# Performance work log

Measured on AMD Instinct MI355X. Metric: run time of the kernel, lower is better.

## Reference

```python
import jax, jax.numpy as jnp
import numpy as np
from jax import lax

# ---- cfg constants (from init_kwargs) ----
MAX_OBS = 10
MAX_AGENTS = 8
MAX_NEI = MAX_AGENTS - 1
A_MAX, W_MAX = 2.0, 1.0
D_MAX, D_OBS, D_SAFE = 5.0, 0.5, 0.8
G_C1, G_C2 = 1.0, 2.0
G_A1, G_A2 = 1.0, 2.0
G_CN1, G_CN2 = 1.0, 2.0
W_SLACK = 100.0
DAMP, STIFF = G_C1 + G_C2, G_C1 * G_C2
DAMP_A, STIFF_A = G_A1 + G_A2, G_A1 * G_A2
DAMP_CN, STIFF_CN = G_CN1 + G_CN2, G_CN1 * G_CN2
NV = 5  # [a, w, delta_obs, delta_agent, delta_conn]
BIG = 1000.0
N_POWER = 30
N_FISTA = 300
B = 32768

PINV = jnp.array([0.5, 0.5, 1.0 / (2.0 * W_SLACK), 1.0 / (2.0 * W_SLACK), 1.0 / (2.0 * W_SLACK)], jnp.float32)


def _build_Gh(v, p_obs, obs_mask, p_agents, v_agents_local, agents_mask, p_c, v_c, c_mask):
    """Build the batched inequality system A x <= b (incl. box constraints)."""
    Bn = v.shape[0]
    f32 = jnp.float32
    # slack non-negativity rows: -delta_k <= 0
    G_slack = jnp.broadcast_to(jnp.array([[0, 0, -1, 0, 0], [0, 0, 0, -1, 0], [0, 0, 0, 0, -1]], f32), (Bn, 3, NV))
    h_slack = jnp.zeros((Bn, 3), f32)
    # obstacle HOCBF rows
    lx, ly = p_obs[..., 0], p_obs[..., 1]            # (B, MAX_OBS)
    h_obs = lx ** 2 + ly ** 2 - D_OBS ** 2
    h_dot = -2.0 * lx * v
    h_rhs = 2.0 * v ** 2 + DAMP * h_dot + STIFF * h_obs
    z = jnp.zeros_like(lx)
    G_obs = jnp.stack([2.0 * lx * obs_mask, 2.0 * ly * v * obs_mask, -obs_mask, z, z], axis=-1)
    h_obs_r = jnp.where(obs_mask > 0, h_rhs, BIG)
    # neighbor avoidance rows
    ax, ay = p_agents[..., 0], p_agents[..., 1]
    vjx, vjy = v_agents_local[..., 0], v_agents_local[..., 1]
    h_av = ax ** 2 + ay ** 2 - D_SAFE ** 2
    h_av_dot = -2.0 * ax * v + 2.0 * (ax * vjx + ay * vjy)
    h_av_dd = 2.0 * v ** 2 - 2.0 * v * vjx + 2.0 * (-v * vjx + vjx ** 2 + vjy ** 2)
    h_rhs_av = h_av_dd + DAMP_A * h_av_dot + STIFF_A * h_av
    za = jnp.zeros_like(ax)
    G_nei = jnp.stack([2.0 * ax * agents_mask,
                       (2.0 * ay * v - 2.0 * ay * vjx + 2.0 * ax * vjy) * agents_mask,
                       za, -agents_mask, za], axis=-1)
    h_nei_r = jnp.where(agents_mask > 0, h_rhs_av, BIG)
    # connectivity row (closest agent)
    cx, cy = p_c[..., 0], p_c[..., 1]                # (B, 1)
    cvx, cvy = v_c[..., 0], v_c[..., 1]
    h_cn = D_MAX ** 2 - (cx ** 2 + cy ** 2)
    h_cn_dot = -(-2.0 * cx * v + 2.0 * (cx * cvx + cy * cvy))
    h_cn_dd = -(2.0 * v ** 2 - 2.0 * v * cvx + 2.0 * (-v * cvx + cvx ** 2 + cvy ** 2))
    h_rhs_cn = h_cn_dd + DAMP_CN * h_cn_dot + STIFF_CN * h_cn
    zc = jnp.zeros_like(cx)
    G_cn = jnp.stack([-2.0 * cx * c_mask,
                      -(2.0 * cy * v - 2.0 * cy * cvx + 2.0 * cx * cvy) * c_mask,
                      zc, zc, -c_mask], axis=-1)
    h_cn_r = jnp.where(c_mask > 0, h_rhs_cn, BIG)
    # leftover unpopulated row (original allocates max_obs+max_agents+1 hocbf rows but fills max_obs+max_nei+1)
    G_extra = jnp.zeros((Bn, 1, NV), f32)
    h_extra = jnp.full((Bn, 1), BIG, f32)
    # box constraints on u (appended as separate cvxpy constraints in the original)
    G_box = jnp.broadcast_to(jnp.array([[-1, 0, 0, 0, 0], [1, 0, 0, 0, 0], [0, -1, 0, 0, 0], [0, 1, 0, 0, 0]], f32), (Bn, 4, NV))
    h_box = jnp.broadcast_to(jnp.array([A_MAX, A_MAX, W_MAX, W_MAX], f32), (Bn, 4))
    A = jnp.concatenate([G_slack, G_obs, G_nei, G_cn, G_extra, G_box], axis=1)
    b = jnp.concatenate([h_slack, h_obs_r, h_nei_r, h_cn_r, h_extra, h_box], axis=1)
    return A, b


def _solve_qp(u_ref, A, b):
    """min ||u-u_ref||^2 + w*sum(delta^2) s.t. A x <= b; solved via dual FISTA.
    P = diag(2,2,2w,2w,2w), q = (-2 u_ref, 0,0,0). x(lam) = -Pinv (q + A^T lam)."""
    Bn = u_ref.shape[0]
    q = jnp.concatenate([-2.0 * u_ref, jnp.zeros((Bn, 3), u_ref.dtype)], axis=1)  # (B,5)
    # Lipschitz constant of dual gradient: ||A Pinv A^T||_2 via power iteration (constant wrt grads)
    Mm = jnp.einsum('bmn,n,bkn->bmk', A, PINV, A)  # (B, M, M), M=26 tiny
    v0 = jnp.ones((Bn, Mm.shape[1]), A.dtype)
    def power(vv, _):
        w = jnp.einsum('bmk,bk->bm', Mm, vv)
        return w / (jnp.linalg.norm(w, axis=1, keepdims=True) + 1e-12), None
    vtop, _ = lax.scan(power, v0, None, length=N_POWER)
    L = jnp.einsum('bm,bmk,bk->b', vtop, Mm, vtop)
    step = lax.stop_gradient(1.0 / (L + 1e-6))[:, None]  # (B,1)

    def x_of(lam_or_y):
        return -(q + jnp.einsum('bmn,bm->bn', A, lam_or_y)) * PINV

    def fista(carry, _):
        lam, y, tk = carry
        resid = jnp.einsum('bmn,bn->bm', A, x_of(y)) - b
        lam_n = jnp.maximum(y + step * resid, 0.0)
        tk1 = 0.5 * (1.0 + jnp.sqrt(1.0 + 4.0 * tk * tk))
        y_n = lam_n + ((tk - 1.0) / tk1) * (lam_n - lam)
        return (lam_n, y_n, tk1), None

    lam0 = jnp.zeros_like(b)
    (lam, _, _), _ = lax.scan(fista, (lam0, lam0, jnp.float32(1.0)), None, length=N_FISTA)
    x = x_of(lam)
    return x[:, :2]  # u_safe


def setup_inputs() -> dict:
    key = jax.random.key(0)
    ks = jax.random.split(key, 8)
    f32 = jnp.float32
    return {
        'u_nominal': jax.random.normal(ks[0], (B, 2), f32),
        'v_current': jax.random.uniform(ks[1], (B, 1), f32),
        'p_obs': 2.0 * jax.random.normal(ks[2], (B, MAX_OBS, 2), f32),
        'obs_mask': jnp.ones((B, MAX_OBS), f32),
        'p_agents': 2.0 * jax.random.normal(ks[3], (B, MAX_NEI, 2), f32),
        'v_agents_local': jax.random.normal(ks[4], (B, MAX_NEI, 2), f32),
        'agents_mask': jnp.ones((B, MAX_NEI), f32),
        'p_c_agent': 2.0 * jax.random.normal(ks[5], (B, 1, 2), f32),
        'v_c_agent': jax.random.normal(ks[6], (B, 1, 2), f32),
        'closest_mask': jnp.ones((B, 1), f32),
    }


def reference(u_nominal, v_current, p_obs, obs_mask, p_agents, v_agents_local, agents_mask, p_c_agent, v_c_agent, closest_mask):
    A, b = _build_Gh(v_current, p_obs, obs_mask, p_agents, v_agents_local, agents_mask, p_c_agent, v_c_agent, closest_mask)
    return _solve_qp(u_nominal, A, b)
```

## Files before the change

kernel.cpp:

```cpp
#include <hip/hip_runtime.h>


typedef float v2f __attribute__((ext_vector_type(2)));

namespace {
constexpr int N_POWER = 30;
constexpr int N_FISTA = 300;
constexpr float PINV_S = 1.0f / 200.0f;
constexpr float BIG = 1000.0f;

constexpr double csqrt(double x) {
    double r = x * 0.5 + 0.5;
    for (int i = 0; i < 50; ++i) r = 0.5 * (r + x / r);
    return r;
}
struct alignas(32) BOct { float b[8]; };
struct BetaTab8 { BOct q[N_FISTA / 4 + 1]; };
constexpr BetaTab8 make_beta8() {
    BetaTab8 t{};
    float tk = 1.0f;
    for (int k = 0; k < N_FISTA; ++k) {
        const float tk1 = 0.5f * (1.0f + (float)csqrt(1.0 + 4.0 * (double)tk * (double)tk));
        const float bb = (tk - 1.0f) / tk1;
        t.q[k / 4].b[(k % 4) * 2]     = bb;
        t.q[k / 4].b[(k % 4) * 2 + 1] = bb;
        tk = tk1;
    }
    return t;
}
}
__constant__ BetaTab8 BETA8 = make_beta8();

template <int CTRL>
__device__ __forceinline__ float dpp_xor_add(float x) {
    int perm = __builtin_amdgcn_mov_dpp(__float_as_int(x), CTRL, 0xF, 0xF, true);
    return x + __int_as_float(perm);
}

__device__ __forceinline__ v2f vfma(v2f a, v2f b, v2f c) {
    return __builtin_elementwise_fma(a, b, c);
}
__device__ __forceinline__ v2f vmax0(v2f a) {
    const v2f z = {0.f, 0.f};
    return __builtin_elementwise_max(a, z);
}

__global__ __launch_bounds__(256, 2) void cbf_fista11(
    const float* __restrict__ u_nom,
    const float* __restrict__ v_cur,
    const float* __restrict__ p_obs,
    const float* __restrict__ obs_mask,
    const float* __restrict__ p_ag,
    const float* __restrict__ v_ag,
    const float* __restrict__ ag_mask,
    const float* __restrict__ p_c,
    const float* __restrict__ v_c,
    const float* __restrict__ c_mask,
    float* __restrict__ out,
    int B)
{
    const int t = blockIdx.x * 256 + threadIdx.x;
    const int p = t >> 2;
    const int sub = t & 3;
    if (p >= B) return;

    const float v  = v_cur[p];
    const float u0 = u_nom[2 * p];
    const float u1 = u_nom[2 * p + 1];

    float r0[6], r1[6], rA[6], nb[6];
#pragma unroll
    for (int s = 0; s < 6; ++s) { r0[s] = 0.f; r1[s] = 0.f; rA[s] = 0.f; nb[s] = -BIG; }

    auto obs_row = [&](int i, int s) {
        const float lx = p_obs[(p * 10 + i) * 2];
        const float ly = p_obs[(p * 10 + i) * 2 + 1];
        const float m  = obs_mask[p * 10 + i];
        const float h   = lx * lx + ly * ly - 0.25f;
        const float hd  = -2.f * lx * v;
        const float rhs = 2.f * v * v + 3.f * hd + 2.f * h;
        r0[s] = 2.f * lx * m;
        r1[s] = 2.f * ly * v * m;
        rA[s] = -m;
        nb[s] = (m > 0.f) ? -rhs : -BIG;
    };
    auto nei_row = [&](int j, int s) {
        const float ax  = p_ag[(p * 7 + j) * 2];
        const float ay  = p_ag[(p * 7 + j) * 2 + 1];
        const float vjx = v_ag[(p * 7 + j) * 2];
        const float vjy = v_ag[(p * 7 + j) * 2 + 1];
        const float m   = ag_mask[p * 7 + j];
        const float h   = ax * ax + ay * ay - 0.64f;
        const float hd  = -2.f * ax * v + 2.f * (ax * vjx + ay * vjy);
        const float hdd = 2.f * v * v - 2.f * v * vjx
                        + 2.f * (-v * vjx + vjx * vjx + vjy * vjy);
        const float rhs = hdd + 3.f * hd + 2.f * h;
        r0[s] = 2.f * ax * m;
        r1[s] = (2.f * ay * v - 2.f * ay * vjx + 2.f * ax * vjy) * m;
        rA[s] = -m;
        nb[s] = (m > 0.f) ? -rhs : -BIG;
    };

    if (sub == 0) {
        obs_row(0, 0); obs_row(1, 1); obs_row(2, 2);
        obs_row(3, 3); obs_row(4, 4); obs_row(5, 5);
    } else if (sub == 1) {
        obs_row(6, 0); obs_row(7, 1); obs_row(8, 2); obs_row(9, 3);
        rA[4] = -1.f; nb[4] = 0.f;
        r0[5] = -1.f; nb[5] = -2.f;
    } else if (sub == 2) {
        nei_row(0, 0); nei_row(1, 1); nei_row(2, 2);
        nei_row(3, 3); nei_row(4, 4); nei_row(5, 5);
    } else {
        nei_row(6, 0);
        rA[1] = -1.f; nb[1] = 0.f;
        r0[2] =  1.f; nb[2] = -2.f;
        r1[3] = -1.f; nb[3] = -1.f;
        r1[4] =  1.f; nb[4] = -1.f;
    }

    v2f R0[3], R1[3], RA[3], NB[3];
#pragma unroll
    for (int k = 0; k < 3; ++k) {
        R0[k] = v2f{r0[2 * k], r0[2 * k + 1]};
        R1[k] = v2f{r1[2 * k], r1[2 * k + 1]};
        RA[k] = v2f{rA[2 * k], rA[2 * k + 1]};
        NB[k] = v2f{nb[2 * k], nb[2 * k + 1]};
    }

    float c0, c1, cB;
    v2f C0v, C1v, CB2, NCBv;
    {
        const float cx  = p_c[2 * p];
        const float cy  = p_c[2 * p + 1];
        const float cvx = v_c[2 * p];
        const float cvy = v_c[2 * p + 1];
        const float m   = c_mask[p];
        const float h   = 25.f - (cx * cx + cy * cy);
        const float hd  = 2.f * cx * v - 2.f * (cx * cvx + cy * cvy);
        const float hdd = -(2.f * v * v - 2.f * v * cvx
                          + 2.f * (-v * cvx + cvx * cvx + cvy * cvy));
        const float rhs = hdd + 3.f * hd + 2.f * h;
        c0 = -2.f * cx * m;
        c1 = -(2.f * cy * v - 2.f * cy * cvx + 2.f * cx * cvy) * m;
        cB = -m;
        const float ncb = (m > 0.f) ? -rhs : -BIG;
        C0v  = v2f{c0, 0.f};
        C1v  = v2f{c1, 0.f};
        CB2  = v2f{cB, -1.f};
        NCBv = v2f{ncb, 0.f};
    }

    v2f PV[3];
#pragma unroll
    for (int k = 0; k < 3; ++k) PV[k] = v2f{1.f, 1.f};
    float pvC = 1.f, pvS = 1.f;

    auto apply_M = [&]() {
        v2f A0 = vfma(R0[0], PV[0], vfma(R0[1], PV[1], R0[2] * PV[2]));
        v2f A1 = vfma(R1[0], PV[0], vfma(R1[1], PV[1], R1[2] * PV[2]));
        v2f AA = vfma(RA[0], PV[0], vfma(RA[1], PV[1], RA[2] * PV[2]));
        float a0 = A0.x + A0.y, a1 = A1.x + A1.y, aA = AA.x + AA.y;
        a0 = dpp_xor_add<0xB1>(a0); a0 = dpp_xor_add<0x4E>(a0);
        a1 = dpp_xor_add<0xB1>(a1); a1 = dpp_xor_add<0x4E>(a1);
        aA = dpp_xor_add<0xB1>(aA);
        a0 = fmaf(c0, pvC, a0);
        a1 = fmaf(c1, pvC, a1);
        const float aC = fmaf(cB, pvC, -pvS);
        const float x0 = 0.5f * a0, x1 = 0.5f * a1;
        const float xA = PINV_S * aA, xC = PINV_S * aC;
        const v2f X0 = {x0, x0}, X1 = {x1, x1}, XA = {xA, xA};
#pragma unroll
        for (int k = 0; k < 3; ++k)
            PV[k] = vfma(R0[k], X0, vfma(R1[k], X1, RA[k] * XA));
        pvC = fmaf(c0, x0, fmaf(c1, x1, cB * xC));
        pvS = -xC;
    };

#pragma unroll 1
    for (int o = 0; o < N_POWER / 2; ++o) {
        apply_M();
        apply_M();
        v2f NS = vfma(PV[0], PV[0], vfma(PV[1], PV[1], PV[2] * PV[2]));
        float nsq = NS.x + NS.y;
        nsq = dpp_xor_add<0xB1>(nsq); nsq = dpp_xor_add<0x4E>(nsq);
        nsq = fmaf(pvC, pvC, fmaf(pvS, pvS, nsq));
        const float inv = __builtin_amdgcn_rsqf(nsq + 1e-24f);
        const v2f INV = {inv, inv};
#pragma unroll
        for (int k = 0; k < 3; ++k) PV[k] = PV[k] * INV;
        pvC *= inv;
        pvS *= inv;
    }
    float nsh, pA;
    {
        v2f A0 = vfma(R0[0], PV[0], vfma(R0[1], PV[1], R0[2] * PV[2]));
        v2f A1 = vfma(R1[0], PV[0], vfma(R1[1], PV[1], R1[2] * PV[2]));
        v2f AA = vfma(RA[0], PV[0], vfma(RA[1], PV[1], RA[2] * PV[2]));
        float a0 = A0.x + A0.y, a1 = A1.x + A1.y, aA = AA.x + AA.y;
        a0 = dpp_xor_add<0xB1>(a0); a0 = dpp_xor_add<0x4E>(a0);
        a1 = dpp_xor_add<0xB1>(a1); a1 = dpp_xor_add<0x4E>(a1);
        aA = dpp_xor_add<0xB1>(aA);
        a0 = fmaf(c0, pvC, a0);
        a1 = fmaf(c1, pvC, a1);
        const float aC = fmaf(cB, pvC, -pvS);
        float tq = aA * aA;
        tq = dpp_xor_add<0x4E>(tq);
        const float L = 0.5f * (a0 * a0 + a1 * a1) + PINV_S * (tq + aC * aC);
        const float step = __builtin_amdgcn_rcpf(L + 1e-6f);
        nsh = -0.5f * step;
        pA  = -PINV_S * step;
    }

    v2f RA2[3];
    {
        const v2f PAv = {pA, pA};
#pragma unroll
        for (int k = 0; k < 3; ++k) RA2[k] = RA[k] * PAv;
    }
    const v2f CB2s = CB2 * v2f{pA, pA};

    v2f LAE[3], LAO[3], ZV[3];
#pragma unroll
    for (int k = 0; k < 3; ++k) {
        LAE[k] = v2f{0.f, 0.f}; LAO[k] = v2f{0.f, 0.f}; ZV[k] = v2f{0.f, 0.f};
    }
    v2f laCSE = {0.f, 0.f}, laCSO = {0.f, 0.f}, zCS = {0.f, 0.f};

    auto half_step = [&](v2f (&ln_)[3], const v2f (&lp_)[3],
                         v2f& lnCS, v2f lpCS, v2f Bv) {
        v2f A0 = vfma(R0[0], ZV[0], vfma(R0[1], ZV[1], R0[2] * ZV[2]));
        v2f A1 = vfma(R1[0], ZV[0], vfma(R1[1], ZV[1], R1[2] * ZV[2]));
        v2f AA = vfma(RA2[0], ZV[0], vfma(RA2[1], ZV[1], RA2[2] * ZV[2]));
        float a0 = A0.x + A0.y, a1 = A1.x + A1.y, aA = AA.x + AA.y;
        a0 = dpp_xor_add<0xB1>(a0); a0 = dpp_xor_add<0x4E>(a0);
        a1 = dpp_xor_add<0xB1>(a1); a1 = dpp_xor_add<0x4E>(a1);
        aA = dpp_xor_add<0xB1>(aA);
        const v2f tCs = CB2s * zCS;
        const float xC = tCs.x + tCs.y;
        const float x0 = fmaf(nsh, fmaf(c0, zCS.x, a0), u0);
        const float x1 = fmaf(nsh, fmaf(c1, zCS.x, a1), u1);
        const v2f X0 = {x0, x0}, X1 = {x1, x1}, XA = {aA, aA}, XC = {xC, xC};
#pragma unroll
        for (int k = 0; k < 3; ++k) {
            const v2f resid = vfma(R0[k], X0, vfma(R1[k], X1, vfma(RA[k], XA, NB[k])));
            const v2f l = vmax0(ZV[k] + resid);
            ZV[k] = vfma(Bv, l - lp_[k], l);
            ln_[k] = l;
        }
        {
            const v2f resid = vfma(C0v, X0, vfma(C1v, X1, vfma(CB2, XC, NCBv)));
            const v2f l = vmax0(zCS + resid);
            zCS = vfma(Bv, l - lpCS, l);
            lnCS = l;
        }
    };

    BOct bo = BETA8.q[0];
#pragma unroll 1
    for (int o = 0; o < N_FISTA / 4; ++o) {
        const BOct bn = BETA8.q[o + 1];
        const v2f B0 = {bo.b[0], bo.b[1]};
        const v2f B1 = {bo.b[2], bo.b[3]};
        const v2f B2 = {bo.b[4], bo.b[5]};
        const v2f B3 = {bo.b[6], bo.b[7]};
        half_step(LAE, LAO, laCSE, laCSO, B0);
        half_step(LAO, LAE, laCSO, laCSE, B1);
        half_step(LAE, LAO, laCSE, laCSO, B2);
        half_step(LAO, LAE, laCSO, laCSE, B3);
        bo = bn;
    }

    v2f A0 = vfma(R0[0], LAO[0], vfma(R0[1], LAO[1], R0[2] * LAO[2]));
    v2f A1 = vfma(R1[0], LAO[0], vfma(R1[1], LAO[1], R1[2] * LAO[2]));
    float a0 = A0.x + A0.y, a1 = A1.x + A1.y;
    a0 = dpp_xor_add<0xB1>(a0); a0 = dpp_xor_add<0x4E>(a0);
    a1 = dpp_xor_add<0xB1>(a1); a1 = dpp_xor_add<0x4E>(a1);
    a0 = fmaf(c0, laCSO.x, a0);
    a1 = fmaf(c1, laCSO.x, a1);
    if (sub == 0) {
        out[2 * p]     = fmaf(nsh, a0, u0);
        out[2 * p + 1] = fmaf(nsh, a1, u1);
    }
}

extern "C" void kernel_launch(void* const* d_in, const int* in_sizes, int n_in,
                              void* d_out, int out_size, void* d_ws, size_t ws_size,
                              hipStream_t stream) {
    const float* u_nom    = (const float*)d_in[0];
    const float* v_cur    = (const float*)d_in[1];
    const float* p_obs    = (const float*)d_in[2];
    const float* obs_mask = (const float*)d_in[3];
    const float* p_ag     = (const float*)d_in[4];
    const float* v_ag     = (const float*)d_in[5];
    const float* ag_mask  = (const float*)d_in[6];
    const float* p_c      = (const float*)d_in[7];
    const float* v_c      = (const float*)d_in[8];
    const float* c_mask   = (const float*)d_in[9];
    float* out = (float*)d_out;

    const int B = in_sizes[0] / 2;
    const long long threads = 4LL * B;
    const int grid = (int)((threads + 255) / 256);
    cbf_fista11<<<grid, 256, 0, stream>>>(
        u_nom, v_cur, p_obs, obs_mask, p_ag, v_ag, ag_mask, p_c, v_c, c_mask, out, B);
}
```

Before: 144.7 us.

## Process two independent QPs per 4-lane group to interleave dependency chains

Each 4-thread group now solves two problems (q and q+half) with their power-iteration and FISTA steps interleaved, halving the grid. The aim is to hide the latency of the serial DPP reductions and FMA chains through instruction-level parallelism across two independent chains. Launch bounds change from 2 to 1 blocks per CU minimum, which lets the compiler use more registers for the doubled state. The risk is fewer resident waves and higher register pressure, which could cancel the ILP benefit.

```diff
diff --git a/kernel.cpp b/kernel.cpp
--- a/kernel.cpp
+++ b/kernel.cpp
@@ -45,28 +45,25 @@
     return __builtin_elementwise_max(a, z);
 }
 
-__global__ __launch_bounds__(256, 2) void cbf_fista11(
-    const float* __restrict__ u_nom,
-    const float* __restrict__ v_cur,
-    const float* __restrict__ p_obs,
-    const float* __restrict__ obs_mask,
-    const float* __restrict__ p_ag,
-    const float* __restrict__ v_ag,
-    const float* __restrict__ ag_mask,
-    const float* __restrict__ p_c,
-    const float* __restrict__ v_c,
-    const float* __restrict__ c_mask,
-    float* __restrict__ out,
-    int B)
-{
-    const int t = blockIdx.x * 256 + threadIdx.x;
-    const int p = t >> 2;
-    const int sub = t & 3;
-    if (p >= B) return;
-
-    const float v  = v_cur[p];
-    const float u0 = u_nom[2 * p];
-    const float u1 = u_nom[2 * p + 1];
+struct Rows {
+    v2f R0[3], R1[3], RA[3], NB[3];
+    v2f C0v, C1v, CB2, NCBv;
+    float c0, c1, cB;
+    float u0, u1;
+};
+
+__device__ __forceinline__ void build_rows(
+    int p, int sub,
+    const float* __restrict__ u_nom, const float* __restrict__ v_cur,
+    const float* __restrict__ p_obs, const float* __restrict__ obs_mask,
+    const float* __restrict__ p_ag,  const float* __restrict__ v_ag,
+    const float* __restrict__ ag_mask, const float* __restrict__ p_c,
+    const float* __restrict__ v_c,   const float* __restrict__ c_mask,
+    Rows& R)
+{
+    const float v = v_cur[p];
+    R.u0 = u_nom[2 * p];
+    R.u1 = u_nom[2 * p + 1];
 
     float r0[6], r1[6], rA[6], nb[6];
 #pragma unroll
@@ -119,17 +116,14 @@
         r1[4] =  1.f; nb[4] = -1.f;
     }
 
-    v2f R0[3], R1[3], RA[3], NB[3];
 #pragma unroll
     for (int k = 0; k < 3; ++k) {
-        R0[k] = v2f{r0[2 * k], r0[2 * k + 1]};
-        R1[k] = v2f{r1[2 * k], r1[2 * k + 1]};
-        RA[k] = v2f{rA[2 * k], rA[2 * k + 1]};
-        NB[k] = v2f{nb[2 * k], nb[2 * k + 1]};
-    }
-
-    float c0, c1, cB;
-    v2f C0v, C1v, CB2, NCBv;
+        R.R0[k] = v2f{r0[2 * k], r0[2 * k + 1]};
+        R.R1[k] = v2f{r1[2 * k], r1[2 * k + 1]};
+        R.RA[k] = v2f{rA[2 * k], rA[2 * k + 1]};
+        R.NB[k] = v2f{nb[2 * k], nb[2 * k + 1]};
+    }
+
     {
         const float cx  = p_c[2 * p];
         const float cy  = p_c[2 * p + 1];
@@ -141,120 +135,177 @@
         const float hdd = -(2.f * v * v - 2.f * v * cvx
                           + 2.f * (-v * cvx + cvx * cvx + cvy * cvy));
         const float rhs = hdd + 3.f * hd + 2.f * h;
-        c0 = -2.f * cx * m;
-        c1 = -(2.f * cy * v - 2.f * cy * cvx + 2.f * cx * cvy) * m;
-        cB = -m;
+        R.c0 = -2.f * cx * m;
+        R.c1 = -(2.f * cy * v - 2.f * cy * cvx + 2.f * cx * cvy) * m;
+        R.cB = -m;
         const float ncb = (m > 0.f) ? -rhs : -BIG;
-        C0v  = v2f{c0, 0.f};
-        C1v  = v2f{c1, 0.f};
-        CB2  = v2f{cB, -1.f};
-        NCBv = v2f{ncb, 0.f};
-    }
-
-    v2f PV[3];
-#pragma unroll
-    for (int k = 0; k < 3; ++k) PV[k] = v2f{1.f, 1.f};
-    float pvC = 1.f, pvS = 1.f;
-
-    auto apply_M = [&]() {
-        v2f A0 = vfma(R0[0], PV[0], vfma(R0[1], PV[1], R0[2] * PV[2]));
-        v2f A1 = vfma(R1[0], PV[0], vfma(R1[1], PV[1], R1[2] * PV[2]));
-        v2f AA = vfma(RA[0], PV[0], vfma(RA[1], PV[1], RA[2] * PV[2]));
-        float a0 = A0.x + A0.y, a1 = A1.x + A1.y, aA = AA.x + AA.y;
-        a0 = dpp_xor_add<0xB1>(a0); a0 = dpp_xor_add<0x4E>(a0);
-        a1 = dpp_xor_add<0xB1>(a1); a1 = dpp_xor_add<0x4E>(a1);
-        aA = dpp_xor_add<0xB1>(aA);
-        a0 = fmaf(c0, pvC, a0);
-        a1 = fmaf(c1, pvC, a1);
-        const float aC = fmaf(cB, pvC, -pvS);
-        const float x0 = 0.5f * a0, x1 = 0.5f * a1;
-        const float xA = PINV_S * aA, xC = PINV_S * aC;
-        const v2f X0 = {x0, x0}, X1 = {x1, x1}, XA = {xA, xA};
-#pragma unroll
-        for (int k = 0; k < 3; ++k)
-            PV[k] = vfma(R0[k], X0, vfma(R1[k], X1, RA[k] * XA));
-        pvC = fmaf(c0, x0, fmaf(c1, x1, cB * xC));
-        pvS = -xC;
-    };
+        R.C0v  = v2f{R.c0, 0.f};
+        R.C1v  = v2f{R.c1, 0.f};
+        R.CB2  = v2f{R.cB, -1.f};
+        R.NCBv = v2f{ncb, 0.f};
+    }
+}
+
+__device__ __forceinline__ void apply_M(const Rows& R, v2f (&PV)[3], float& pvC, float& pvS)
+{
+    v2f A0 = vfma(R.R0[0], PV[0], vfma(R.R0[1], PV[1], R.R0[2] * PV[2]));
+    v2f A1 = vfma(R.R1[0], PV[0], vfma(R.R1[1], PV[1], R.R1[2] * PV[2]));
+    v2f AA = vfma(R.RA[0], PV[0], vfma(R.RA[1], PV[1], R.RA[2] * PV[2]));
+    float a0 = A0.x + A0.y, a1 = A1.x + A1.y, aA = AA.x + AA.y;
+    a0 = dpp_xor_add<0xB1>(a0); a0 = dpp_xor_add<0x4E>(a0);
+    a1 = dpp_xor_add<0xB1>(a1); a1 = dpp_xor_add<0x4E>(a1);
+    aA = dpp_xor_add<0xB1>(aA);
+    a0 = fmaf(R.c0, pvC, a0);
+    a1 = fmaf(R.c1, pvC, a1);
+    const float aC = fmaf(R.cB, pvC, -pvS);
+    const float x0 = 0.5f * a0, x1 = 0.5f * a1;
+    const float xA = PINV_S * aA, xC = PINV_S * aC;
+    const v2f X0 = {x0, x0}, X1 = {x1, x1}, XA = {xA, xA};
+#pragma unroll
+    for (int k = 0; k < 3; ++k)
+        PV[k] = vfma(R.R0[k], X0, vfma(R.R1[k], X1, R.RA[k] * XA));
+    pvC = fmaf(R.c0, x0, fmaf(R.c1, x1, R.cB * xC));
+    pvS = -xC;
+}
+
+__device__ __forceinline__ void pnorm(v2f (&PV)[3], float& pvC, float& pvS)
+{
+    v2f NS = vfma(PV[0], PV[0], vfma(PV[1], PV[1], PV[2] * PV[2]));
+    float nsq = NS.x + NS.y;
+    nsq = dpp_xor_add<0xB1>(nsq); nsq = dpp_xor_add<0x4E>(nsq);
+    nsq = fmaf(pvC, pvC, fmaf(pvS, pvS, nsq));
+    const float inv = __builtin_amdgcn_rsqf(nsq + 1e-24f);
+    const v2f INV = {inv, inv};
+#pragma unroll
+    for (int k = 0; k < 3; ++k) PV[k] = PV[k] * INV;
+    pvC *= inv;
+    pvS *= inv;
+}
+
+__device__ __forceinline__ void step_consts(const Rows& R, const v2f (&PV)[3],
+                                            float pvC, float pvS,
+                                            float& nsh, float& pA)
+{
+    v2f A0 = vfma(R.R0[0], PV[0], vfma(R.R0[1], PV[1], R.R0[2] * PV[2]));
+    v2f A1 = vfma(R.R1[0], PV[0], vfma(R.R1[1], PV[1], R.R1[2] * PV[2]));
+    v2f AA = vfma(R.RA[0], PV[0], vfma(R.RA[1], PV[1], R.RA[2] * PV[2]));
+    float a0 = A0.x + A0.y, a1 = A1.x + A1.y, aA = AA.x + AA.y;
+    a0 = dpp_xor_add<0xB1>(a0); a0 = dpp_xor_add<0x4E>(a0);
+    a1 = dpp_xor_add<0xB1>(a1); a1 = dpp_xor_add<0x4E>(a1);
+    aA = dpp_xor_add<0xB1>(aA);
+    a0 = fmaf(R.c0, pvC, a0);
+    a1 = fmaf(R.c1, pvC, a1);
+    const float aC = fmaf(R.cB, pvC, -pvS);
+    float tq = aA * aA;
+    tq = dpp_xor_add<0x4E>(tq);
+    const float L = 0.5f * (a0 * a0 + a1 * a1) + PINV_S * (tq + aC * aC);
+    const float step = __builtin_amdgcn_rcpf(L + 1e-6f);
+    nsh = -0.5f * step;
+    pA  = -PINV_S * step;
+}
+
+__device__ __forceinline__ void half_step(const Rows& R, const v2f (&RA2)[3], v2f CB2s,
+                                          float nsh,
+                                          v2f (&ZV)[3], v2f& zCS,
+                                          v2f (&ln)[3], const v2f (&lp)[3],
+                                          v2f& lnCS, v2f lpCS, v2f Bv)
+{
+    v2f A0 = vfma(R.R0[0], ZV[0], vfma(R.R0[1], ZV[1], R.R0[2] * ZV[2]));
+    v2f A1 = vfma(R.R1[0], ZV[0], vfma(R.R1[1], ZV[1], R.R1[2] * ZV[2]));
+    v2f AA = vfma(RA2[0], ZV[0], vfma(RA2[1], ZV[1], RA2[2] * ZV[2]));
+    float a0 = A0.x + A0.y, a1 = A1.x + A1.y, aA = AA.x + AA.y;
+    a0 = dpp_xor_add<0xB1>(a0); a0 = dpp_xor_add<0x4E>(a0);
+    a1 = dpp_xor_add<0xB1>(a1); a1 = dpp_xor_add<0x4E>(a1);
+    aA = dpp_xor_add<0xB1>(aA);
+    const v2f tCs = CB2s * zCS;
+    const float xC = tCs.x + tCs.y;
+    const float x0 = fmaf(nsh, fmaf(R.c0, zCS.x, a0), R.u0);
+    const float x1 = fmaf(nsh, fmaf(R.c1, zCS.x, a1), R.u1);
+    const v2f X0 = {x0, x0}, X1 = {x1, x1}, XA = {aA, aA}, XC = {xC, xC};
+#pragma unroll
+    for (int k = 0; k < 3; ++k) {
+        const v2f resid = vfma(R.R0[k], X0, vfma(R.R1[k], X1, vfma(R.RA[k], XA, R.NB[k])));
+        const v2f l = vmax0(ZV[k] + resid);
+        ZV[k] = vfma(Bv, l - lp[k], l);
+        ln[k] = l;
+    }
+    {
+        const v2f resid = vfma(R.C0v, X0, vfma(R.C1v, X1, vfma(R.CB2, XC, R.NCBv)));
+        const v2f l = vmax0(zCS + resid);
+        zCS = vfma(Bv, l - lpCS, l);
+        lnCS = l;
+    }
+}
+
+struct Fst {
+    v2f LAE[3], LAO[3], ZV[3];
+    v2f laCSE, laCSO, zCS;
+};
+
+__global__ __launch_bounds__(256, 1) void cbf_fista12(
+    const float* __restrict__ u_nom,
+    const float* __restrict__ v_cur,
+    const float* __restrict__ p_obs,
+    const float* __restrict__ obs_mask,
+    const float* __restrict__ p_ag,
+    const float* __restrict__ v_ag,
+    const float* __restrict__ ag_mask,
+    const float* __restrict__ p_c,
+    const float* __restrict__ v_c,
+    const float* __restrict__ c_mask,
+    float* __restrict__ out,
+    int B)
+{
+    const int t = blockIdx.x * 256 + threadIdx.x;
+    const int q = t >> 2;
+    const int sub = t & 3;
+    const int half = (B + 1) >> 1;
+    if (q >= half) return;
+
+    const int pa = q;
+    const int pbi = q + half;
+    const bool hasB = (pbi < B);
+    const int pb = hasB ? pbi : pa;
+
+    Rows Ra, Rb;
+    build_rows(pa, sub, u_nom, v_cur, p_obs, obs_mask, p_ag, v_ag, ag_mask, p_c, v_c, c_mask, Ra);
+    build_rows(pb, sub, u_nom, v_cur, p_obs, obs_mask, p_ag, v_ag, ag_mask, p_c, v_c, c_mask, Rb);
+
+    v2f PVa[3], PVb[3];
+#pragma unroll
+    for (int k = 0; k < 3; ++k) { PVa[k] = v2f{1.f, 1.f}; PVb[k] = v2f{1.f, 1.f}; }
+    float pvCa = 1.f, pvSa = 1.f, pvCb = 1.f, pvSb = 1.f;
 
 #pragma unroll 1
     for (int o = 0; o < N_POWER / 2; ++o) {
-        apply_M();
-        apply_M();
-        v2f NS = vfma(PV[0], PV[0], vfma(PV[1], PV[1], PV[2] * PV[2]));
-        float nsq = NS.x + NS.y;
-        nsq = dpp_xor_add<0xB1>(nsq); nsq = dpp_xor_add<0x4E>(nsq);
-        nsq = fmaf(pvC, pvC, fmaf(pvS, pvS, nsq));
-        const float inv = __builtin_amdgcn_rsqf(nsq + 1e-24f);
-        const v2f INV = {inv, inv};
-#pragma unroll
-        for (int k = 0; k < 3; ++k) PV[k] = PV[k] * INV;
-        pvC *= inv;
-        pvS *= inv;
-    }
-    float nsh, pA;
-    {
-        v2f A0 = vfma(R0[0], PV[0], vfma(R0[1], PV[1], R0[2] * PV[2]));
-        v2f A1 = vfma(R1[0], PV[0], vfma(R1[1], PV[1], R1[2] * PV[2]));
-        v2f AA = vfma(RA[0], PV[0], vfma(RA[1], PV[1], RA[2] * PV[2]));
-        float a0 = A0.x + A0.y, a1 = A1.x + A1.y, aA = AA.x + AA.y;
-        a0 = dpp_xor_add<0xB1>(a0); a0 = dpp_xor_add<0x4E>(a0);
-        a1 = dpp_xor_add<0xB1>(a1); a1 = dpp_xor_add<0x4E>(a1);
-        aA = dpp_xor_add<0xB1>(aA);
-        a0 = fmaf(c0, pvC, a0);
-        a1 = fmaf(c1, pvC, a1);
-        const float aC = fmaf(cB, pvC, -pvS);
-        float tq = aA * aA;
-        tq = dpp_xor_add<0x4E>(tq);
-        const float L = 0.5f * (a0 * a0 + a1 * a1) + PINV_S * (tq + aC * aC);
-        const float step = __builtin_amdgcn_rcpf(L + 1e-6f);
-        nsh = -0.5f * step;
-        pA  = -PINV_S * step;
-    }
-
-    v2f RA2[3];
-    {
-        const v2f PAv = {pA, pA};
-#pragma unroll
-        for (int k = 0; k < 3; ++k) RA2[k] = RA[k] * PAv;
-    }
-    const v2f CB2s = CB2 * v2f{pA, pA};
-
-    v2f LAE[3], LAO[3], ZV[3];
+        apply_M(Ra, PVa, pvCa, pvSa);
+        apply_M(Rb, PVb, pvCb, pvSb);
+        apply_M(Ra, PVa, pvCa, pvSa);
+        apply_M(Rb, PVb, pvCb, pvSb);
+        pnorm(PVa, pvCa, pvSa);
+        pnorm(PVb, pvCb, pvSb);
+    }
+    float nsha, pAa, nshb, pAb;
+    step_consts(Ra, PVa, pvCa, pvSa, nsha, pAa);
+    step_consts(Rb, PVb, pvCb, pvSb, nshb, pAb);
+
+    v2f RA2a[3], RA2b[3];
 #pragma unroll
     for (int k = 0; k < 3; ++k) {
-        LAE[k] = v2f{0.f, 0.f}; LAO[k] = v2f{0.f, 0.f}; ZV[k] = v2f{0.f, 0.f};
-    }
-    v2f laCSE = {0.f, 0.f}, laCSO = {0.f, 0.f}, zCS = {0.f, 0.f};
-
-    auto half_step = [&](v2f (&ln_)[3], const v2f (&lp_)[3],
-                         v2f& lnCS, v2f lpCS, v2f Bv) {
-        v2f A0 = vfma(R0[0], ZV[0], vfma(R0[1], ZV[1], R0[2] * ZV[2]));
-        v2f A1 = vfma(R1[0], ZV[0], vfma(R1[1], ZV[1], R1[2] * ZV[2]));
-        v2f AA = vfma(RA2[0], ZV[0], vfma(RA2[1], ZV[1], RA2[2] * ZV[2]));
-        float a0 = A0.x + A0.y, a1 = A1.x + A1.y, aA = AA.x + AA.y;
-        a0 = dpp_xor_add<0xB1>(a0); a0 = dpp_xor_add<0x4E>(a0);
-        a1 = dpp_xor_add<0xB1>(a1); a1 = dpp_xor_add<0x4E>(a1);
-        aA = dpp_xor_add<0xB1>(aA);
-        const v2f tCs = CB2s * zCS;
-        const float xC = tCs.x + tCs.y;
-        const float x0 = fmaf(nsh, fmaf(c0, zCS.x, a0), u0);
-        const float x1 = fmaf(nsh, fmaf(c1, zCS.x, a1), u1);
-        const v2f X0 = {x0, x0}, X1 = {x1, x1}, XA = {aA, aA}, XC = {xC, xC};
-#pragma unroll
-        for (int k = 0; k < 3; ++k) {
-            const v2f resid = vfma(R0[k], X0, vfma(R1[k], X1, vfma(RA[k], XA, NB[k])));
-            const v2f l = vmax0(ZV[k] + resid);
-            ZV[k] = vfma(Bv, l - lp_[k], l);
-            ln_[k] = l;
-        }
-        {
-            const v2f resid = vfma(C0v, X0, vfma(C1v, X1, vfma(CB2, XC, NCBv)));
-            const v2f l = vmax0(zCS + resid);
-            zCS = vfma(Bv, l - lpCS, l);
-            lnCS = l;
-        }
-    };
+        RA2a[k] = Ra.RA[k] * v2f{pAa, pAa};
+        RA2b[k] = Rb.RA[k] * v2f{pAb, pAb};
+    }
+    const v2f CB2sa = Ra.CB2 * v2f{pAa, pAa};
+    const v2f CB2sb = Rb.CB2 * v2f{pAb, pAb};
+
+    Fst Sa, Sb;
+#pragma unroll
+    for (int k = 0; k < 3; ++k) {
+        Sa.LAE[k] = v2f{0.f, 0.f}; Sa.LAO[k] = v2f{0.f, 0.f}; Sa.ZV[k] = v2f{0.f, 0.f};
+        Sb.LAE[k] = v2f{0.f, 0.f}; Sb.LAO[k] = v2f{0.f, 0.f}; Sb.ZV[k] = v2f{0.f, 0.f};
+    }
+    Sa.laCSE = v2f{0.f, 0.f}; Sa.laCSO = v2f{0.f, 0.f}; Sa.zCS = v2f{0.f, 0.f};
+    Sb.laCSE = v2f{0.f, 0.f}; Sb.laCSO = v2f{0.f, 0.f}; Sb.zCS = v2f{0.f, 0.f};
 
     BOct bo = BETA8.q[0];
 #pragma unroll 1
@@ -264,23 +315,42 @@
         const v2f B1 = {bo.b[2], bo.b[3]};
         const v2f B2 = {bo.b[4], bo.b[5]};
         const v2f B3 = {bo.b[6], bo.b[7]};
-        half_step(LAE, LAO, laCSE, laCSO, B0);
-        half_step(LAO, LAE, laCSO, laCSE, B1);
-        half_step(LAE, LAO, laCSE, laCSO, B2);
-        half_step(LAO, LAE, laCSO, laCSE, B3);
+        half_step(Ra, RA2a, CB2sa, nsha, Sa.ZV, Sa.zCS, Sa.LAE, Sa.LAO, Sa.laCSE, Sa.laCSO, B0);
+        half_step(Rb, RA2b, CB2sb, nshb, Sb.ZV, Sb.zCS, Sb.LAE, Sb.LAO, Sb.laCSE, Sb.laCSO, B0);
+        half_step(Ra, RA2a, CB2sa, nsha, Sa.ZV, Sa.zCS, Sa.LAO, Sa.LAE, Sa.laCSO, Sa.laCSE, B1);
+        half_step(Rb, RA2b, CB2sb, nshb, Sb.ZV, Sb.zCS, Sb.LAO, Sb.LAE, Sb.laCSO, Sb.laCSE, B1);
+        half_step(Ra, RA2a, CB2sa, nsha, Sa.ZV, Sa.zCS, Sa.LAE, Sa.LAO, Sa.laCSE, Sa.laCSO, B2);
+        half_step(Rb, RA2b, CB2sb, nshb, Sb.ZV, Sb.zCS, Sb.LAE, Sb.LAO, Sb.laCSE, Sb.laCSO, B2);
+        half_step(Ra, RA2a, CB2sa, nsha, Sa.ZV, Sa.zCS, Sa.LAO, Sa.LAE, Sa.laCSO, Sa.laCSE, B3);
+        half_step(Rb, RA2b, CB2sb, nshb, Sb.ZV, Sb.zCS, Sb.LAO, Sb.LAE, Sb.laCSO, Sb.laCSE, B3);
         bo = bn;
     }
 
-    v2f A0 = vfma(R0[0], LAO[0], vfma(R0[1], LAO[1], R0[2] * LAO[2]));
-    v2f A1 = vfma(R1[0], LAO[0], vfma(R1[1], LAO[1], R1[2] * LAO[2]));
-    float a0 = A0.x + A0.y, a1 = A1.x + A1.y;
-    a0 = dpp_xor_add<0xB1>(a0); a0 = dpp_xor_add<0x4E>(a0);
-    a1 = dpp_xor_add<0xB1>(a1); a1 = dpp_xor_add<0x4E>(a1);
-    a0 = fmaf(c0, laCSO.x, a0);
-    a1 = fmaf(c1, laCSO.x, a1);
-    if (sub == 0) {
-        out[2 * p]     = fmaf(nsh, a0, u0);
-        out[2 * p + 1] = fmaf(nsh, a1, u1);
+    {
+        v2f A0 = vfma(Ra.R0[0], Sa.LAO[0], vfma(Ra.R0[1], Sa.LAO[1], Ra.R0[2] * Sa.LAO[2]));
+        v2f A1 = vfma(Ra.R1[0], Sa.LAO[0], vfma(Ra.R1[1], Sa.LAO[1], Ra.R1[2] * Sa.LAO[2]));
+        float a0 = A0.x + A0.y, a1 = A1.x + A1.y;
+        a0 = dpp_xor_add<0xB1>(a0); a0 = dpp_xor_add<0x4E>(a0);
+        a1 = dpp_xor_add<0xB1>(a1); a1 = dpp_xor_add<0x4E>(a1);
+        a0 = fmaf(Ra.c0, Sa.laCSO.x, a0);
+        a1 = fmaf(Ra.c1, Sa.laCSO.x, a1);
+        if (sub == 0) {
+            out[2 * pa]     = fmaf(nsha, a0, Ra.u0);
+            out[2 * pa + 1] = fmaf(nsha, a1, Ra.u1);
+        }
+    }
+    {
+        v2f A0 = vfma(Rb.R0[0], Sb.LAO[0], vfma(Rb.R0[1], Sb.LAO[1], Rb.R0[2] * Sb.LAO[2]));
+        v2f A1 = vfma(Rb.R1[0], Sb.LAO[0], vfma(Rb.R1[1], Sb.LAO[1], Rb.R1[2] * Sb.LAO[2]));
+        float a0 = A0.x + A0.y, a1 = A1.x + A1.y;
+        a0 = dpp_xor_add<0xB1>(a0); a0 = dpp_xor_add<0x4E>(a0);
+        a1 = dpp_xor_add<0xB1>(a1); a1 = dpp_xor_add<0x4E>(a1);
+        a0 = fmaf(Rb.c0, Sb.laCSO.x, a0);
+        a1 = fmaf(Rb.c1, Sb.laCSO.x, a1);
+        if (sub == 0 && hasB) {
+            out[2 * pbi]     = fmaf(nshb, a0, Rb.u0);
+            out[2 * pbi + 1] = fmaf(nshb, a1, Rb.u1);
+        }
     }
 }
 
@@ -300,8 +370,9 @@
     float* out = (float*)d_out;
 
     const int B = in_sizes[0] / 2;
-    const long long threads = 4LL * B;
+    const int half = (B + 1) / 2;
+    const long long threads = 4LL * half;
     const int grid = (int)((threads + 255) / 256);
-    cbf_fista11<<<grid, 256, 0, stream>>>(
+    cbf_fista12<<<grid, 256, 0, stream>>>(
         u_nom, v_cur, p_obs, obs_mask, p_ag, v_ag, ag_mask, p_c, v_c, c_mask, out, B);
 }
```

New measurement: 162.9 us. +12.6%, slower.

## Pack two problems per thread group into v2f lanes instead of row pairs

Applied to the files above, without the earlier changes.

Changes the packed-float layout so each lane of a v2f holds a different QP problem (problem q and q+half), with 6 rows per thread held as scalar-per-problem, halving the thread count. The in-register x/y horizontal add is removed and the DPP reductions are now done per problem. The connectivity and its slack row also become separate v2f states, and launch bounds drop to 1 block per SM. The intent is better packed-math utilization and fewer redundant per-thread ops, at the cost of more registers, fewer waves in flight and duplicated DPP reductions.

```diff
diff --git a/kernel.cpp b/kernel.cpp
--- a/kernel.cpp
+++ b/kernel.cpp
@@ -36,6 +36,9 @@
     int perm = __builtin_amdgcn_mov_dpp(__float_as_int(x), CTRL, 0xF, 0xF, true);
     return x + __int_as_float(perm);
 }
+__device__ __forceinline__ float dpp2(float x) {
+    return dpp_xor_add<0x4E>(dpp_xor_add<0xB1>(x));
+}
 
 __device__ __forceinline__ v2f vfma(v2f a, v2f b, v2f c) {
     return __builtin_elementwise_fma(a, b, c);
@@ -44,31 +47,29 @@
     const v2f z = {0.f, 0.f};
     return __builtin_elementwise_max(a, z);
 }
-
-__global__ __launch_bounds__(256, 2) void cbf_fista11(
-    const float* __restrict__ u_nom,
-    const float* __restrict__ v_cur,
-    const float* __restrict__ p_obs,
-    const float* __restrict__ obs_mask,
-    const float* __restrict__ p_ag,
-    const float* __restrict__ v_ag,
-    const float* __restrict__ ag_mask,
-    const float* __restrict__ p_c,
-    const float* __restrict__ v_c,
-    const float* __restrict__ c_mask,
-    float* __restrict__ out,
-    int B)
+__device__ __forceinline__ v2f tree6(const v2f (&C)[6], const v2f (&Z)[6]) {
+    v2f s0 = vfma(C[1], Z[1], C[0] * Z[0]);
+    s0 = vfma(C[2], Z[2], s0);
+    v2f s1 = vfma(C[4], Z[4], C[3] * Z[3]);
+    s1 = vfma(C[5], Z[5], s1);
+    return s0 + s1;
+}
+
+struct ConnS { float c0, c1, cB, ncb, u0, u1; };
+
+__device__ __forceinline__ void build_scalar(
+    int p, int sub,
+    const float* __restrict__ u_nom, const float* __restrict__ v_cur,
+    const float* __restrict__ p_obs, const float* __restrict__ obs_mask,
+    const float* __restrict__ p_ag,  const float* __restrict__ v_ag,
+    const float* __restrict__ ag_mask, const float* __restrict__ p_c,
+    const float* __restrict__ v_c,   const float* __restrict__ c_mask,
+    float (&r0)[6], float (&r1)[6], float (&rA)[6], float (&nb)[6], ConnS& cs)
 {
-    const int t = blockIdx.x * 256 + threadIdx.x;
-    const int p = t >> 2;
-    const int sub = t & 3;
-    if (p >= B) return;
-
-    const float v  = v_cur[p];
-    const float u0 = u_nom[2 * p];
-    const float u1 = u_nom[2 * p + 1];
-
-    float r0[6], r1[6], rA[6], nb[6];
+    const float v = v_cur[p];
+    cs.u0 = u_nom[2 * p];
+    cs.u1 = u_nom[2 * p + 1];
+
 #pragma unroll
     for (int s = 0; s < 6; ++s) { r0[s] = 0.f; r1[s] = 0.f; rA[s] = 0.f; nb[s] = -BIG; }
 
@@ -119,17 +120,6 @@
         r1[4] =  1.f; nb[4] = -1.f;
     }
 
-    v2f R0[3], R1[3], RA[3], NB[3];
-#pragma unroll
-    for (int k = 0; k < 3; ++k) {
-        R0[k] = v2f{r0[2 * k], r0[2 * k + 1]};
-        R1[k] = v2f{r1[2 * k], r1[2 * k + 1]};
-        RA[k] = v2f{rA[2 * k], rA[2 * k + 1]};
-        NB[k] = v2f{nb[2 * k], nb[2 * k + 1]};
-    }
-
-    float c0, c1, cB;
-    v2f C0v, C1v, CB2, NCBv;
     {
         const float cx  = p_c[2 * p];
         const float cy  = p_c[2 * p + 1];
@@ -141,39 +131,83 @@
         const float hdd = -(2.f * v * v - 2.f * v * cvx
                           + 2.f * (-v * cvx + cvx * cvx + cvy * cvy));
         const float rhs = hdd + 3.f * hd + 2.f * h;
-        c0 = -2.f * cx * m;
-        c1 = -(2.f * cy * v - 2.f * cy * cvx + 2.f * cx * cvy) * m;
-        cB = -m;
-        const float ncb = (m > 0.f) ? -rhs : -BIG;
-        C0v  = v2f{c0, 0.f};
-        C1v  = v2f{c1, 0.f};
-        CB2  = v2f{cB, -1.f};
-        NCBv = v2f{ncb, 0.f};
-    }
-
-    v2f PV[3];
-#pragma unroll
-    for (int k = 0; k < 3; ++k) PV[k] = v2f{1.f, 1.f};
-    float pvC = 1.f, pvS = 1.f;
+        cs.c0 = -2.f * cx * m;
+        cs.c1 = -(2.f * cy * v - 2.f * cy * cvx + 2.f * cx * cvy) * m;
+        cs.cB = -m;
+        cs.ncb = (m > 0.f) ? -rhs : -BIG;
+    }
+}
+
+__global__ __launch_bounds__(256, 1) void cbf_fista13(
+    const float* __restrict__ u_nom,
+    const float* __restrict__ v_cur,
+    const float* __restrict__ p_obs,
+    const float* __restrict__ obs_mask,
+    const float* __restrict__ p_ag,
+    const float* __restrict__ v_ag,
+    const float* __restrict__ ag_mask,
+    const float* __restrict__ p_c,
+    const float* __restrict__ v_c,
+    const float* __restrict__ c_mask,
+    float* __restrict__ out,
+    int B)
+{
+    const int t = blockIdx.x * 256 + threadIdx.x;
+    const int q = t >> 2;
+    const int sub = t & 3;
+    const int half = (B + 1) >> 1;
+    if (q >= half) return;
+
+    const int pa = q;
+    const int pbi = q + half;
+    const bool hasB = (pbi < B);
+    const int pb = hasB ? pbi : pa;
+
+    float r0a[6], r1a[6], rAa[6], nba[6]; ConnS ca;
+    float r0b[6], r1b[6], rAb[6], nbb[6]; ConnS cb;
+    build_scalar(pa, sub, u_nom, v_cur, p_obs, obs_mask, p_ag, v_ag, ag_mask, p_c, v_c, c_mask,
+                 r0a, r1a, rAa, nba, ca);
+    build_scalar(pb, sub, u_nom, v_cur, p_obs, obs_mask, p_ag, v_ag, ag_mask, p_c, v_c, c_mask,
+                 r0b, r1b, rAb, nbb, cb);
+
+    v2f R0[6], R1[6], RA[6], NB[6];
+#pragma unroll
+    for (int k = 0; k < 6; ++k) {
+        R0[k] = v2f{r0a[k], r0b[k]};
+        R1[k] = v2f{r1a[k], r1b[k]};
+        RA[k] = v2f{rAa[k], rAb[k]};
+        NB[k] = v2f{nba[k], nbb[k]};
+    }
+    const v2f c0p  = {ca.c0,  cb.c0};
+    const v2f c1p  = {ca.c1,  cb.c1};
+    const v2f cBp  = {ca.cB,  cb.cB};
+    const v2f ncbp = {ca.ncb, cb.ncb};
+    const v2f u0p  = {ca.u0,  cb.u0};
+    const v2f u1p  = {ca.u1,  cb.u1};
+
+    v2f PV[6];
+#pragma unroll
+    for (int k = 0; k < 6; ++k) PV[k] = v2f{1.f, 1.f};
+    v2f pvC = {1.f, 1.f}, pvS = {1.f, 1.f};
 
     auto apply_M = [&]() {
-        v2f A0 = vfma(R0[0], PV[0], vfma(R0[1], PV[1], R0[2] * PV[2]));
-        v2f A1 = vfma(R1[0], PV[0], vfma(R1[1], PV[1], R1[2] * PV[2]));
-        v2f AA = vfma(RA[0], PV[0], vfma(RA[1], PV[1], RA[2] * PV[2]));
-        float a0 = A0.x + A0.y, a1 = A1.x + A1.y, aA = AA.x + AA.y;
-        a0 = dpp_xor_add<0xB1>(a0); a0 = dpp_xor_add<0x4E>(a0);
-        a1 = dpp_xor_add<0xB1>(a1); a1 = dpp_xor_add<0x4E>(a1);
-        aA = dpp_xor_add<0xB1>(aA);
-        a0 = fmaf(c0, pvC, a0);
-        a1 = fmaf(c1, pvC, a1);
-        const float aC = fmaf(cB, pvC, -pvS);
-        const float x0 = 0.5f * a0, x1 = 0.5f * a1;
-        const float xA = PINV_S * aA, xC = PINV_S * aC;
-        const v2f X0 = {x0, x0}, X1 = {x1, x1}, XA = {xA, xA};
-#pragma unroll
-        for (int k = 0; k < 3; ++k)
-            PV[k] = vfma(R0[k], X0, vfma(R1[k], X1, RA[k] * XA));
-        pvC = fmaf(c0, x0, fmaf(c1, x1, cB * xC));
+        const v2f A0 = tree6(R0, PV);
+        const v2f A1 = tree6(R1, PV);
+        const v2f AA = tree6(RA, PV);
+        const float a0A = dpp2(A0.x), a0B = dpp2(A0.y);
+        const float a1A = dpp2(A1.x), a1B = dpp2(A1.y);
+        const float aAA = dpp_xor_add<0xB1>(AA.x);
+        const float aAB = dpp_xor_add<0xB1>(AA.y);
+        const v2f a0p = vfma(c0p, pvC, v2f{a0A, a0B});
+        const v2f a1p = vfma(c1p, pvC, v2f{a1A, a1B});
+        const v2f aCp = vfma(cBp, pvC, -pvS);
+        const v2f x0 = a0p * 0.5f, x1 = a1p * 0.5f;
+        const v2f xA = v2f{aAA, aAB} * PINV_S;
+        const v2f xC = aCp * PINV_S;
+#pragma unroll
+        for (int k = 0; k < 6; ++k)
+            PV[k] = vfma(R0[k], x0, vfma(R1[k], x1, RA[k] * xA));
+        pvC = vfma(c0p, x0, vfma(c1p, x1, cBp * xC));
         pvS = -xC;
     };
 
@@ -181,78 +215,87 @@
     for (int o = 0; o < N_POWER / 2; ++o) {
         apply_M();
         apply_M();
-        v2f NS = vfma(PV[0], PV[0], vfma(PV[1], PV[1], PV[2] * PV[2]));
-        float nsq = NS.x + NS.y;
-        nsq = dpp_xor_add<0xB1>(nsq); nsq = dpp_xor_add<0x4E>(nsq);
-        nsq = fmaf(pvC, pvC, fmaf(pvS, pvS, nsq));
-        const float inv = __builtin_amdgcn_rsqf(nsq + 1e-24f);
-        const v2f INV = {inv, inv};
-#pragma unroll
-        for (int k = 0; k < 3; ++k) PV[k] = PV[k] * INV;
-        pvC *= inv;
-        pvS *= inv;
-    }
-    float nsh, pA;
+        const v2f NS = tree6(PV, PV);
+        const float nA = dpp2(NS.x), nB = dpp2(NS.y);
+        const v2f nsq = vfma(pvC, pvC, vfma(pvS, pvS, v2f{nA, nB}));
+        const float invA = __builtin_amdgcn_rsqf(nsq.x + 1e-24f);
+        const float invB = __builtin_amdgcn_rsqf(nsq.y + 1e-24f);
+        const v2f INV = {invA, invB};
+#pragma unroll
+        for (int k = 0; k < 6; ++k) PV[k] = PV[k] * INV;
+        pvC = pvC * INV;
+        pvS = pvS * INV;
+    }
+
+    v2f nsh_p, pA_p;
     {
-        v2f A0 = vfma(R0[0], PV[0], vfma(R0[1], PV[1], R0[2] * PV[2]));
-        v2f A1 = vfma(R1[0], PV[0], vfma(R1[1], PV[1], R1[2] * PV[2]));
-        v2f AA = vfma(RA[0], PV[0], vfma(RA[1], PV[1], RA[2] * PV[2]));
-        float a0 = A0.x + A0.y, a1 = A1.x + A1.y, aA = AA.x + AA.y;
-        a0 = dpp_xor_add<0xB1>(a0); a0 = dpp_xor_add<0x4E>(a0);
-        a1 = dpp_xor_add<0xB1>(a1); a1 = dpp_xor_add<0x4E>(a1);
-        aA = dpp_xor_add<0xB1>(aA);
-        a0 = fmaf(c0, pvC, a0);
-        a1 = fmaf(c1, pvC, a1);
-        const float aC = fmaf(cB, pvC, -pvS);
-        float tq = aA * aA;
-        tq = dpp_xor_add<0x4E>(tq);
-        const float L = 0.5f * (a0 * a0 + a1 * a1) + PINV_S * (tq + aC * aC);
-        const float step = __builtin_amdgcn_rcpf(L + 1e-6f);
-        nsh = -0.5f * step;
-        pA  = -PINV_S * step;
-    }
-
-    v2f RA2[3];
-    {
-        const v2f PAv = {pA, pA};
-#pragma unroll
-        for (int k = 0; k < 3; ++k) RA2[k] = RA[k] * PAv;
-    }
-    const v2f CB2s = CB2 * v2f{pA, pA};
-
-    v2f LAE[3], LAO[3], ZV[3];
-#pragma unroll
-    for (int k = 0; k < 3; ++k) {
-        LAE[k] = v2f{0.f, 0.f}; LAO[k] = v2f{0.f, 0.f}; ZV[k] = v2f{0.f, 0.f};
-    }
-    v2f laCSE = {0.f, 0.f}, laCSO = {0.f, 0.f}, zCS = {0.f, 0.f};
-
-    auto half_step = [&](v2f (&ln_)[3], const v2f (&lp_)[3],
-                         v2f& lnCS, v2f lpCS, v2f Bv) {
-        v2f A0 = vfma(R0[0], ZV[0], vfma(R0[1], ZV[1], R0[2] * ZV[2]));
-        v2f A1 = vfma(R1[0], ZV[0], vfma(R1[1], ZV[1], R1[2] * ZV[2]));
-        v2f AA = vfma(RA2[0], ZV[0], vfma(RA2[1], ZV[1], RA2[2] * ZV[2]));
-        float a0 = A0.x + A0.y, a1 = A1.x + A1.y, aA = AA.x + AA.y;
-        a0 = dpp_xor_add<0xB1>(a0); a0 = dpp_xor_add<0x4E>(a0);
-        a1 = dpp_xor_add<0xB1>(a1); a1 = dpp_xor_add<0x4E>(a1);
-        aA = dpp_xor_add<0xB1>(aA);
-        const v2f tCs = CB2s * zCS;
-        const float xC = tCs.x + tCs.y;
-        const float x0 = fmaf(nsh, fmaf(c0, zCS.x, a0), u0);
-        const float x1 = fmaf(nsh, fmaf(c1, zCS.x, a1), u1);
-        const v2f X0 = {x0, x0}, X1 = {x1, x1}, XA = {aA, aA}, XC = {xC, xC};
-#pragma unroll
-        for (int k = 0; k < 3; ++k) {
+        const v2f A0 = tree6(R0, PV);
+        const v2f A1 = tree6(R1, PV);
+        const v2f AA = tree6(RA, PV);
+        const float a0A = dpp2(A0.x), a0B = dpp2(A0.y);
+        const float a1A = dpp2(A1.x), a1B = dpp2(A1.y);
+        const float aAA = dpp_xor_add<0xB1>(AA.x);
+        const float aAB = dpp_xor_add<0xB1>(AA.y);
+        const v2f a0p = vfma(c0p, pvC, v2f{a0A, a0B});
+        const v2f a1p = vfma(c1p, pvC, v2f{a1A, a1B});
+        const v2f aCp = vfma(cBp, pvC, -pvS);
+        const v2f aAp = {aAA, aAB};
+        const v2f sq = aAp * aAp;
+        const float tqA = dpp_xor_add<0x4E>(sq.x);
+        const float tqB = dpp_xor_add<0x4E>(sq.y);
+        const v2f tq = vfma(aCp, aCp, v2f{tqA, tqB});
+        const v2f hterm = vfma(a0p, a0p, a1p * a1p) * 0.5f;
+        const v2f L = vfma(tq, v2f{PINV_S, PINV_S}, hterm);
+        const float stA = __builtin_amdgcn_rcpf(L.x + 1e-6f);
+        const float stB = __builtin_amdgcn_rcpf(L.y + 1e-6f);
+        nsh_p = v2f{stA, stB} * -0.5f;
+        pA_p  = v2f{stA, stB} * -PINV_S;
+    }
+
+    v2f RA2[6];
+#pragma unroll
+    for (int k = 0; k < 6; ++k) RA2[k] = RA[k] * pA_p;
+    const v2f cBs = cBp * pA_p;
+    const v2f npA = -pA_p;
+
+    v2f ZV[6], LAE[6], LAO[6];
+#pragma unroll
+    for (int k = 0; k < 6; ++k) {
+        ZV[k] = v2f{0.f, 0.f}; LAE[k] = v2f{0.f, 0.f}; LAO[k] = v2f{0.f, 0.f};
+    }
+    v2f zC = {0.f, 0.f}, zS = {0.f, 0.f};
+    v2f lCE = {0.f, 0.f}, lCO = {0.f, 0.f}, lSE = {0.f, 0.f}, lSO = {0.f, 0.f};
+
+    auto half_step = [&](v2f (&ln)[6], const v2f (&lp)[6],
+                         v2f& lnC, v2f lpC, v2f& lnS, v2f lpS, v2f Bv) {
+        const v2f A0 = tree6(R0, ZV);
+        const v2f A1 = tree6(R1, ZV);
+        const v2f AA = tree6(RA2, ZV);
+        const float a0A = dpp2(A0.x), a0B = dpp2(A0.y);
+        const float a1A = dpp2(A1.x), a1B = dpp2(A1.y);
+        const float xAA = dpp_xor_add<0xB1>(AA.x);
+        const float xAB = dpp_xor_add<0xB1>(AA.y);
+        const v2f XA = {xAA, xAB};
+        const v2f xC = vfma(cBs, zC, npA * zS);
+        const v2f X0 = vfma(nsh_p, vfma(c0p, zC, v2f{a0A, a0B}), u0p);
+        const v2f X1 = vfma(nsh_p, vfma(c1p, zC, v2f{a1A, a1B}), u1p);
+#pragma unroll
+        for (int k = 0; k < 6; ++k) {
             const v2f resid = vfma(R0[k], X0, vfma(R1[k], X1, vfma(RA[k], XA, NB[k])));
             const v2f l = vmax0(ZV[k] + resid);
-            ZV[k] = vfma(Bv, l - lp_[k], l);
-            ln_[k] = l;
+            ZV[k] = vfma(Bv, l - lp[k], l);
+            ln[k] = l;
         }
         {
-            const v2f resid = vfma(C0v, X0, vfma(C1v, X1, vfma(CB2, XC, NCBv)));
-            const v2f l = vmax0(zCS + resid);
-            zCS = vfma(Bv, l - lpCS, l);
-            lnCS = l;
+            const v2f residC = vfma(c0p, X0, vfma(c1p, X1, vfma(cBp, xC, ncbp)));
+            const v2f l = vmax0(zC + residC);
+            zC = vfma(Bv, l - lpC, l);
+            lnC = l;
+        }
+        {
+            const v2f l = vmax0(zS - xC);
+            zS = vfma(Bv, l - lpS, l);
+            lnS = l;
         }
     };
 
@@ -260,27 +303,30 @@
 #pragma unroll 1
     for (int o = 0; o < N_FISTA / 4; ++o) {
         const BOct bn = BETA8.q[o + 1];
-        const v2f B0 = {bo.b[0], bo.b[1]};
-        const v2f B1 = {bo.b[2], bo.b[3]};
-        const v2f B2 = {bo.b[4], bo.b[5]};
-        const v2f B3 = {bo.b[6], bo.b[7]};
-        half_step(LAE, LAO, laCSE, laCSO, B0);
-        half_step(LAO, LAE, laCSO, laCSE, B1);
-        half_step(LAE, LAO, laCSE, laCSO, B2);
-        half_step(LAO, LAE, laCSO, laCSE, B3);
+        half_step(LAE, LAO, lCE, lCO, lSE, lSO, v2f{bo.b[0], bo.b[1]});
+        half_step(LAO, LAE, lCO, lCE, lSO, lSE, v2f{bo.b[2], bo.b[3]});
+        half_step(LAE, LAO, lCE, lCO, lSE, lSO, v2f{bo.b[4], bo.b[5]});
+        half_step(LAO, LAE, lCO, lCE, lSO, lSE, v2f{bo.b[6], bo.b[7]});
         bo = bn;
     }
 
-    v2f A0 = vfma(R0[0], LAO[0], vfma(R0[1], LAO[1], R0[2] * LAO[2]));
-    v2f A1 = vfma(R1[0], LAO[0], vfma(R1[1], LAO[1], R1[2] * LAO[2]));
-    float a0 = A0.x + A0.y, a1 = A1.x + A1.y;
-    a0 = dpp_xor_add<0xB1>(a0); a0 = dpp_xor_add<0x4E>(a0);
-    a1 = dpp_xor_add<0xB1>(a1); a1 = dpp_xor_add<0x4E>(a1);
-    a0 = fmaf(c0, laCSO.x, a0);
-    a1 = fmaf(c1, laCSO.x, a1);
-    if (sub == 0) {
-        out[2 * p]     = fmaf(nsh, a0, u0);
-        out[2 * p + 1] = fmaf(nsh, a1, u1);
+    {
+        const v2f A0 = tree6(R0, LAO);
+        const v2f A1 = tree6(R1, LAO);
+        const float a0A = dpp2(A0.x), a0B = dpp2(A0.y);
+        const float a1A = dpp2(A1.x), a1B = dpp2(A1.y);
+        const v2f a0p = vfma(c0p, lCO, v2f{a0A, a0B});
+        const v2f a1p = vfma(c1p, lCO, v2f{a1A, a1B});
+        const v2f o0 = vfma(nsh_p, a0p, u0p);
+        const v2f o1 = vfma(nsh_p, a1p, u1p);
+        if (sub == 0) {
+            out[2 * pa]     = o0.x;
+            out[2 * pa + 1] = o1.x;
+            if (hasB) {
+                out[2 * pbi]     = o0.y;
+                out[2 * pbi + 1] = o1.y;
+            }
+        }
     }
 }
 
@@ -300,8 +346,9 @@
     float* out = (float*)d_out;
 
     const int B = in_sizes[0] / 2;
-    const long long threads = 4LL * B;
+    const int half = (B + 1) / 2;
+    const long long threads = 4LL * half;
     const int grid = (int)((threads + 255) / 256);
-    cbf_fista11<<<grid, 256, 0, stream>>>(
+    cbf_fista13<<<grid, 256, 0, stream>>>(
         u_nom, v_cur, p_obs, obs_mask, p_ag, v_ag, ag_mask, p_c, v_c, c_mask, out, B);
 }
```

After: 144.1 us. Within noise of the previous version (-0.4%).
